# Optimization experiments

Hardware: AMD Instinct MI355X
Metric: run time of the kernel (lower is better)

The kernel has to match this reference:

```python
import jax, jax.numpy as jnp
import numpy as np

L, D, H, FF = 4, 1024, 16, 4096
DH = D // H
EPS = 1e-5


def _ln(x, w, b):
    m = jnp.mean(x, axis=-1, keepdims=True)
    v = jnp.mean(jnp.square(x - m), axis=-1, keepdims=True)
    return (x - m) * jax.lax.rsqrt(v + EPS) * w + b


def setup_inputs() -> dict:
    key = jax.random.key(0)
    ks = jax.random.split(key, 16)
    s = 0.02
    inp = {
        "x": jax.random.normal(ks[0], (2, 2048, D), dtype=jnp.float32),
        "Wq": jax.random.normal(ks[1], (L, D, D), dtype=jnp.float32) * s,
        "Wk": jax.random.normal(ks[2], (L, D, D), dtype=jnp.float32) * s,
        "Wv": jax.random.normal(ks[3], (L, D, D), dtype=jnp.float32) * s,
        "Wo": jax.random.normal(ks[4], (L, D, D), dtype=jnp.float32) * s,
        "bq": jnp.zeros((L, D), jnp.float32),
        "bk": jnp.zeros((L, D), jnp.float32),
        "bv": jnp.zeros((L, D), jnp.float32),
        "bo": jnp.zeros((L, D), jnp.float32),
        "W1": jax.random.normal(ks[5], (L, D, FF), dtype=jnp.float32) * s,
        "b1": jnp.zeros((L, FF), jnp.float32),
        "W2": jax.random.normal(ks[6], (L, FF, D), dtype=jnp.float32) * s,
        "b2": jnp.zeros((L, D), jnp.float32),
        "ln1_w": jnp.ones((L, D), jnp.float32),
        "ln1_b": jnp.zeros((L, D), jnp.float32),
        "ln2_w": jnp.ones((L, D), jnp.float32),
        "ln2_b": jnp.zeros((L, D), jnp.float32),
        "lnf_w": jnp.ones((D,), jnp.float32),
        "lnf_b": jnp.zeros((D,), jnp.float32),
    }
    return inp


def reference(x, Wq, Wk, Wv, Wo, bq, bk, bv, bo, W1, b1, W2, b2,
              ln1_w, ln1_b, ln2_w, ln2_b, lnf_w, lnf_b):
    B, S, _ = x.shape
    scale = 1.0 / jnp.sqrt(jnp.float32(DH))
    for i in range(L):
        # --- pre-norm self-attention (naive math SDPA) ---
        h = _ln(x, ln1_w[i], ln1_b[i])
        q = (h @ Wq[i] + bq[i]).reshape(B, S, H, DH)
        k = (h @ Wk[i] + bk[i]).reshape(B, S, H, DH)
        v = (h @ Wv[i] + bv[i]).reshape(B, S, H, DH)
        scores = jnp.einsum("bqhd,bkhd->bhqk", q, k) * scale  # [B,H,S,S]
        attn = jax.nn.softmax(scores, axis=-1)
        o = jnp.einsum("bhqk,bkhd->bqhd", attn, v).reshape(B, S, D)
        x = x + (o @ Wo[i] + bo[i])
        # --- pre-norm FFN (ReLU) ---
        h2 = _ln(x, ln2_w[i], ln2_b[i])
        x = x + (jax.nn.relu(h2 @ W1[i] + b1[i]) @ W2[i] + b2[i])
    return _ln(x, lnf_w, lnf_b)
```

## Files before the change

kernel.cpp:

```cpp
#include <hip/hip_runtime.h>
#include <cstddef>
#include <cstdint>


#define D_MODEL 1024
#define FF_DIM  4096
#define NTOK    4096
#define SEQ     2048
#define LLAYERS 4

using short8v = __attribute__((ext_vector_type(8))) short;
using f32x16  = __attribute__((ext_vector_type(16))) float;

#define FMA4(a_, s_, b_) { (a_).x += (s_)*(b_).x; (a_).y += (s_)*(b_).y; \
                           (a_).z += (s_)*(b_).z; (a_).w += (s_)*(b_).w; }

__device__ __forceinline__ unsigned short f2bf(float x) {
  unsigned int u = __float_as_uint(x);
  unsigned int r = u + 0x7fffu + ((u >> 16) & 1u);
  return (unsigned short)(r >> 16);
}
__device__ __forceinline__ float bf2f(unsigned short h) {
  return __uint_as_float(((unsigned int)h) << 16);
}
__device__ __forceinline__ void split2(float x, short& hi, short& lo) {
  unsigned short h = f2bf(x);
  hi = (short)h;
  lo = (short)f2bf(x - bf2f(h));
}

__device__ __forceinline__ void gload16(const short* g, short* l) {
  __builtin_amdgcn_global_load_lds(
      (const __attribute__((address_space(1))) unsigned int*)g,
      (__attribute__((address_space(3))) unsigned int*)l, 16, 0, 0);
}

template<int HILO>
__global__ __launch_bounds__(256)
void ln_k(const float* __restrict__ in, const float* __restrict__ w,
          const float* __restrict__ bia, float* __restrict__ outf,
          short* __restrict__ oh, short* __restrict__ ol)
{
  const int wv = threadIdx.x >> 6, lane = threadIdx.x & 63;
  const size_t row = (size_t)blockIdx.x * 4 + wv;
  const float4* x4 = reinterpret_cast<const float4*>(in + row * D_MODEL);
  float4 v[4];
  float s = 0.f;
#pragma unroll
  for (int i = 0; i < 4; i++) {
    v[i] = x4[lane + 64 * i];
    s += v[i].x + v[i].y + v[i].z + v[i].w;
  }
#pragma unroll
  for (int o = 32; o > 0; o >>= 1) s += __shfl_xor(s, o);
  const float mean = s * (1.f / D_MODEL);
  float qv = 0.f;
#pragma unroll
  for (int i = 0; i < 4; i++) {
    float a = v[i].x - mean, b = v[i].y - mean, c = v[i].z - mean, d = v[i].w - mean;
    qv += a * a + b * b + c * c + d * d;
  }
#pragma unroll
  for (int o = 32; o > 0; o >>= 1) qv += __shfl_xor(qv, o);
  const float rstd = rsqrtf(qv * (1.f / D_MODEL) + 1e-5f);
  const float4* w4 = reinterpret_cast<const float4*>(w);
  const float4* b4 = reinterpret_cast<const float4*>(bia);
#pragma unroll
  for (int i = 0; i < 4; i++) {
    float4 ww = w4[lane + 64 * i], bb = b4[lane + 64 * i], r;
    r.x = (v[i].x - mean) * rstd * ww.x + bb.x;
    r.y = (v[i].y - mean) * rstd * ww.y + bb.y;
    r.z = (v[i].z - mean) * rstd * ww.z + bb.z;
    r.w = (v[i].w - mean) * rstd * ww.w + bb.w;
    if (HILO) {
      short4 h, l;
      split2(r.x, h.x, l.x); split2(r.y, h.y, l.y);
      split2(r.z, h.z, l.z); split2(r.w, h.w, l.w);
      size_t off = row * D_MODEL + 4 * lane + 256 * i;
      *reinterpret_cast<short4*>(oh + off) = h;
      *reinterpret_cast<short4*>(ol + off) = l;
    } else {
      reinterpret_cast<float4*>(outf + row * D_MODEL)[lane + 64 * i] = r;
    }
  }
}

struct WPack {
  const float* src[6];
  short* dhi[6];
  short* dlo[6];
  int K[6], N[6];
};
__global__ __launch_bounds__(256)
void cvtw_k(WPack p)
{
  __shared__ float t[32][36];
  const int b = blockIdx.x;
  int m, tile;
  if (b < 4096)      { m = b >> 10; tile = b & 1023; }
  else if (b < 8192) { m = 4; tile = b - 4096; }
  else               { m = 5; tile = b - 8192; }
  const int K = p.K[m], N = p.N[m];
  const int sh = (m == 4) ? 7 : 5;
  const int k0 = (tile >> sh) * 32, n0 = (tile & ((1 << sh) - 1)) * 32;
  const int r = threadIdx.x >> 3, c4 = (threadIdx.x & 7) << 2;
  float4 v = *reinterpret_cast<const float4*>(p.src[m] + (size_t)(k0 + r) * N + n0 + c4);
  *reinterpret_cast<float4*>(&t[r][c4]) = v;
  __syncthreads();
  short4 h, l;
  split2(t[c4 + 0][r], h.x, l.x);
  split2(t[c4 + 1][r], h.y, l.y);
  split2(t[c4 + 2][r], h.z, l.z);
  split2(t[c4 + 3][r], h.w, l.w);
  size_t off = (size_t)(n0 + r) * K + k0 + c4;
  *reinterpret_cast<short4*>(p.dhi[m] + off) = h;
  *reinterpret_cast<short4*>(p.dlo[m] + off) = l;
}

template<int MODE>
__global__ __launch_bounds__(256, 2)
void mgemm_k(const short* __restrict__ Ahg, const short* __restrict__ Alg,
             int K, int Ncols,
             const short* __restrict__ Wh0, const short* __restrict__ Wl0,
             const short* __restrict__ Wh1, const short* __restrict__ Wl1,
             const short* __restrict__ Wh2, const short* __restrict__ Wl2,
             const float* __restrict__ B0, const float* __restrict__ B1,
             const float* __restrict__ B2,
             float* __restrict__ O0, float* __restrict__ O1, float* __restrict__ O2,
             short* __restrict__ OhA, short* __restrict__ OlA,
             short* __restrict__ OhB, short* __restrict__ OlB,
             short* __restrict__ OhC, short* __restrict__ OlC,
             int nbn_per, const float* __restrict__ resid)
{
  __shared__ short Ash0[128 * 64];
  __shared__ short Ash1[128 * 64];
  __shared__ short Bsh0[128 * 64];
  __shared__ short Bsh1[128 * 64];
  const int tid = threadIdx.x;
  const int split = blockIdx.x / nbn_per;
  const int bn = (blockIdx.x % nbn_per) * 128;
  const int bm = blockIdx.y * 128;
  const short* Wh = split == 0 ? Wh0 : (split == 1 ? Wh1 : Wh2);
  const short* Wl = split == 0 ? Wl0 : (split == 1 ? Wl1 : Wl2);
  const float* Bi = split == 0 ? B0 : (split == 1 ? B1 : B2);
  float* Of       = split == 0 ? O0 : (split == 1 ? O1 : O2);
  const int l = tid & 63, w = tid >> 6;
  const int wr = w >> 1, wc = w & 1;

  short* sarr = (w == 0) ? Ash0 : (w == 1) ? Ash1 : (w == 2) ? Bsh0 : Bsh1;
  const short* gbase =
      (w == 0) ? Ahg + (size_t)bm * K :
      (w == 1) ? Alg + (size_t)bm * K :
      (w == 2) ? Wh + (size_t)bn * K :
                 Wl + (size_t)bn * K;
  const int loff = (l >> 3) * K + (((l & 7) ^ (l >> 3)) << 3);

  f32x16 acc[2][2];
#pragma unroll
  for (int a = 0; a < 2; a++)
#pragma unroll
    for (int b = 0; b < 2; b++)
#pragma unroll
      for (int i = 0; i < 16; i++) acc[a][b][i] = 0.f;

  for (int k0 = 0; k0 < K; k0 += 64) {
#pragma unroll
    for (int u = 0; u < 16; u++)
      gload16(gbase + k0 + u * 8 * K + loff, &sarr[u * 512]);
    __syncthreads();
#pragma unroll
    for (int ks = 0; ks < 4; ks++) {
      const int slot = (ks << 1) | (l >> 5);
      short8v afh[2], afl[2], bfh[2], bfl[2];
#pragma unroll
      for (int rt = 0; rt < 2; rt++) {
        int row = wr * 64 + rt * 32 + (l & 31);
        int ia = row * 64 + ((slot ^ (row & 7)) << 3);
        afh[rt] = *reinterpret_cast<const short8v*>(&Ash0[ia]);
        afl[rt] = *reinterpret_cast<const short8v*>(&Ash1[ia]);
        int col = wc * 64 + rt * 32 + (l & 31);
        int ib = col * 64 + ((slot ^ (col & 7)) << 3);
        bfh[rt] = *reinterpret_cast<const short8v*>(&Bsh0[ib]);
        bfl[rt] = *reinterpret_cast<const short8v*>(&Bsh1[ib]);
      }
#pragma unroll
      for (int rt = 0; rt < 2; rt++)
#pragma unroll
        for (int ct = 0; ct < 2; ct++) {
          acc[rt][ct] = __builtin_amdgcn_mfma_f32_32x32x16_bf16(afh[rt], bfh[ct], acc[rt][ct], 0, 0, 0);
          acc[rt][ct] = __builtin_amdgcn_mfma_f32_32x32x16_bf16(afh[rt], bfl[ct], acc[rt][ct], 0, 0, 0);
          acc[rt][ct] = __builtin_amdgcn_mfma_f32_32x32x16_bf16(afl[rt], bfh[ct], acc[rt][ct], 0, 0, 0);
        }
    }
    __syncthreads();
  }

  const int rbase = (l >> 5) * 4, cl = l & 31;
#pragma unroll
  for (int rt = 0; rt < 2; rt++)
#pragma unroll
    for (int ct = 0; ct < 2; ct++) {
      const int colg = bn + wc * 64 + ct * 32 + cl;
      const float bia = Bi[colg];
#pragma unroll
      for (int reg = 0; reg < 16; reg++) {
        const int rowg = bm + wr * 64 + rt * 32 + rbase + (reg & 3) + ((reg >> 2) << 3);
        float v = acc[rt][ct][reg] + bia;
        const size_t off = (size_t)rowg * Ncols + colg;
        if (MODE == 0) {
          Of[off] = v;
        } else if (MODE == 1) {
          Of[off] = v + resid[off];
        } else if (MODE == 2) {
          v = fmaxf(v, 0.f);
          short h, lo; split2(v, h, lo);
          OhA[off] = h; OlA[off] = lo;
        } else {
          short h, lo; split2(v, h, lo);
          if (split < 2) {
            short* OH = split == 0 ? OhA : OhB;
            short* OL = split == 0 ? OlA : OlB;
            OH[off] = h; OL[off] = lo;
          } else {
            const int bbv = rowg >> 11, s = rowg & 2047;
            const int hdv = colg >> 6, dv = colg & 63;
            const int m = s & 15;
            const int pos = (m & 3) + ((m >> 3) << 2) + (((m >> 2) & 1) << 3);
            const size_t voff = ((size_t)(bbv * 16 + hdv) * 64 + dv) * SEQ + (s - m + pos);
            OhC[voff] = h; OlC[voff] = lo;
          }
        }
      }
    }
}

__global__ __launch_bounds__(256)
void mattn_k(const short* __restrict__ qh, const short* __restrict__ ql,
             const short* __restrict__ kh, const short* __restrict__ kl,
             const short* __restrict__ vth, const short* __restrict__ vtl,
             short* __restrict__ oh, short* __restrict__ ol)
{
  __shared__ short Kh[64 * 64], Kl[64 * 64], Vh[64 * 64], Vl[64 * 64];
  const int tid = threadIdx.x;
  const int l = tid & 63, wv = tid >> 6;
  const int lq = l & 31, hb = l >> 5;
  const int qt = blockIdx.x, bh = blockIdx.y;
  const int bb = bh >> 4, hd = bh & 15;

  const size_t qoff = (size_t)(bb * SEQ + qt * 128 + wv * 32 + lq) * D_MODEL + hd * 64 + 8 * hb;
  short8v qfh[4], qfl[4];
#pragma unroll
  for (int c = 0; c < 4; c++) {
    qfh[c] = *reinterpret_cast<const short8v*>(qh + qoff + 16 * c);
    qfl[c] = *reinterpret_cast<const short8v*>(ql + qoff + 16 * c);
  }

  int dst[2];
  size_t kga[2], vga[2];
#pragma unroll
  for (int c = 0; c < 2; c++) {
    int g = tid + c * 256;
    int rr = g >> 3, ss = g & 7;
    dst[c] = rr * 64 + ((ss ^ (rr & 7)) << 3);
    kga[c] = (size_t)(bb * SEQ + rr) * D_MODEL + hd * 64 + ss * 8;
    vga[c] = (size_t)(bh * 64 + rr) * SEQ + ss * 8;
  }
  short8v skh[2], skl[2], svh[2], svl[2];
#pragma unroll
  for (int c = 0; c < 2; c++) {
    skh[c] = *reinterpret_cast<const short8v*>(kh + kga[c]);
    skl[c] = *reinterpret_cast<const short8v*>(kl + kga[c]);
    svh[c] = *reinterpret_cast<const short8v*>(vth + vga[c]);
    svl[c] = *reinterpret_cast<const short8v*>(vtl + vga[c]);
  }

  f32x16 accO[2];
#pragma unroll
  for (int t = 0; t < 2; t++)
#pragma unroll
    for (int i = 0; i < 16; i++) accO[t][i] = 0.f;
  float mrun = -3e38f, lrun = 0.f;

  for (int kt = 0; kt < 32; kt++) {
#pragma unroll
    for (int c = 0; c < 2; c++) {
      *reinterpret_cast<short8v*>(&Kh[dst[c]]) = skh[c];
      *reinterpret_cast<short8v*>(&Kl[dst[c]]) = skl[c];
      *reinterpret_cast<short8v*>(&Vh[dst[c]]) = svh[c];
      *reinterpret_cast<short8v*>(&Vl[dst[c]]) = svl[c];
    }
    __syncthreads();
    if (kt < 31) {
#pragma unroll
      for (int c = 0; c < 2; c++) {
        size_t ko = kga[c] + (size_t)(kt + 1) * 64 * D_MODEL;
        size_t vo = vga[c] + (size_t)(kt + 1) * 64;
        skh[c] = *reinterpret_cast<const short8v*>(kh + ko);
        skl[c] = *reinterpret_cast<const short8v*>(kl + ko);
        svh[c] = *reinterpret_cast<const short8v*>(vth + vo);
        svl[c] = *reinterpret_cast<const short8v*>(vtl + vo);
      }
    }

    f32x16 sc[2];
#pragma unroll
    for (int t = 0; t < 2; t++)
#pragma unroll
      for (int i = 0; i < 16; i++) sc[t][i] = 0.f;
    __builtin_amdgcn_s_setprio(1);
#pragma unroll
    for (int t = 0; t < 2; t++) {
      const int row = 32 * t + lq;
#pragma unroll
      for (int c = 0; c < 4; c++) {
        const int idx = row * 64 + (((2 * c + hb) ^ (row & 7)) << 3);
        short8v ah = *reinterpret_cast<const short8v*>(&Kh[idx]);
        short8v al = *reinterpret_cast<const short8v*>(&Kl[idx]);
        sc[t] = __builtin_amdgcn_mfma_f32_32x32x16_bf16(ah, qfh[c], sc[t], 0, 0, 0);
        sc[t] = __builtin_amdgcn_mfma_f32_32x32x16_bf16(ah, qfl[c], sc[t], 0, 0, 0);
        sc[t] = __builtin_amdgcn_mfma_f32_32x32x16_bf16(al, qfh[c], sc[t], 0, 0, 0);
      }
    }
    __builtin_amdgcn_s_setprio(0);

    float p[2][16];
    float tm = -3e38f;
#pragma unroll
    for (int t = 0; t < 2; t++)
#pragma unroll
      for (int r = 0; r < 16; r++) {
        p[t][r] = sc[t][r] * 0.125f;
        tm = fmaxf(tm, p[t][r]);
      }
    tm = fmaxf(tm, __shfl_xor(tm, 32));
    const float mnew = fmaxf(mrun, tm);
    const float alpha = __expf(mrun - mnew);
    float ps = 0.f;
#pragma unroll
    for (int t = 0; t < 2; t++)
#pragma unroll
      for (int r = 0; r < 16; r++) {
        p[t][r] = __expf(p[t][r] - mnew);
        ps += p[t][r];
      }
    ps += __shfl_xor(ps, 32);
    lrun = lrun * alpha + ps;
    mrun = mnew;
#pragma unroll
    for (int t = 0; t < 2; t++)
#pragma unroll
      for (int i = 0; i < 16; i++) accO[t][i] *= alpha;

    short8v ph[4], pl[4];
#pragma unroll
    for (int c = 0; c < 4; c++) {
#pragma unroll
      for (int j = 0; j < 8; j++) {
        const float v = p[c >> 1][8 * (c & 1) + j];
        const unsigned short hh2 = f2bf(v);
        ph[c][j] = (short)hh2;
        pl[c][j] = (short)f2bf(v - bf2f(hh2));
      }
    }

    __builtin_amdgcn_s_setprio(1);
#pragma unroll
    for (int t = 0; t < 2; t++) {
      const int row = 32 * t + lq;
#pragma unroll
      for (int c = 0; c < 4; c++) {
        const int idx = row * 64 + (((2 * c + hb) ^ (row & 7)) << 3);
        short8v vhf = *reinterpret_cast<const short8v*>(&Vh[idx]);
        short8v vlf = *reinterpret_cast<const short8v*>(&Vl[idx]);
        accO[t] = __builtin_amdgcn_mfma_f32_32x32x16_bf16(vhf, ph[c], accO[t], 0, 0, 0);
        accO[t] = __builtin_amdgcn_mfma_f32_32x32x16_bf16(vhf, pl[c], accO[t], 0, 0, 0);
        accO[t] = __builtin_amdgcn_mfma_f32_32x32x16_bf16(vlf, ph[c], accO[t], 0, 0, 0);
      }
    }
    __builtin_amdgcn_s_setprio(0);
    __syncthreads();
  }

  const float inv = 1.f / lrun;
  const size_t obase = (size_t)(bb * SEQ + qt * 128 + wv * 32 + lq) * D_MODEL + hd * 64;
#pragma unroll
  for (int t = 0; t < 2; t++)
#pragma unroll
    for (int r = 0; r < 16; r++) {
      const int d = 32 * t + (r & 3) + ((r >> 2) << 3) + 4 * hb;
      short hh2, ll2;
      split2(accO[t][r] * inv, hh2, ll2);
      oh[obase + d] = hh2;
      ol[obase + d] = ll2;
    }
}

template<bool RELU, bool RES>
__global__ __launch_bounds__(256)
void gemm_k(const float* __restrict__ A, int K, int Ncols,
            const float* __restrict__ W0, const float* __restrict__ W1p,
            const float* __restrict__ W2p,
            const float* __restrict__ B0, const float* __restrict__ B1p,
            const float* __restrict__ B2p,
            float* __restrict__ O0, float* __restrict__ O1p, float* __restrict__ O2p,
            int nbn_per, const float* __restrict__ resid)
{
  __shared__ float As[16][132];
  __shared__ float Bs[16][132];
  const int tid = threadIdx.x;
  const int split = blockIdx.x / nbn_per;
  const int bn = (blockIdx.x % nbn_per) * 128;
  const int bm = blockIdx.y * 128;
  const float* W  = split == 0 ? W0 : (split == 1 ? W1p : W2p);
  const float* Bi = split == 0 ? B0 : (split == 1 ? B1p : B2p);
  float* O        = split == 0 ? O0 : (split == 1 ? O1p : O2p);
  const int tx = tid & 15, ty = tid >> 4;

  float4 acc[2][4][2];
#pragma unroll
  for (int a = 0; a < 2; a++)
#pragma unroll
    for (int b = 0; b < 4; b++)
#pragma unroll
      for (int c = 0; c < 2; c++) acc[a][b][c] = make_float4(0.f, 0.f, 0.f, 0.f);

  for (int k0 = 0; k0 < K; k0 += 16) {
#pragma unroll
    for (int i = 0; i < 2; i++) {
      int p = tid + i * 256;
      int row = p >> 2, kk4 = (p & 3) << 2;
      float4 va = *reinterpret_cast<const float4*>(A + (size_t)(bm + row) * K + k0 + kk4);
      As[kk4 + 0][row] = va.x; As[kk4 + 1][row] = va.y;
      As[kk4 + 2][row] = va.z; As[kk4 + 3][row] = va.w;
    }
#pragma unroll
    for (int i = 0; i < 2; i++) {
      int p = tid + i * 256;
      int row = p >> 5, c4 = (p & 31) << 2;
      *reinterpret_cast<float4*>(&Bs[row][c4]) =
          *reinterpret_cast<const float4*>(W + (size_t)(k0 + row) * Ncols + bn + c4);
    }
    __syncthreads();
#pragma unroll
    for (int kk = 0; kk < 16; kk++) {
      float4 a0 = *reinterpret_cast<const float4*>(&As[kk][ty * 4]);
      float4 a1 = *reinterpret_cast<const float4*>(&As[kk][64 + ty * 4]);
      float4 b0 = *reinterpret_cast<const float4*>(&Bs[kk][tx * 4]);
      float4 b1 = *reinterpret_cast<const float4*>(&Bs[kk][64 + tx * 4]);
      float av0[4] = {a0.x, a0.y, a0.z, a0.w};
      float av1[4] = {a1.x, a1.y, a1.z, a1.w};
#pragma unroll
      for (int j = 0; j < 4; j++) {
        FMA4(acc[0][j][0], av0[j], b0); FMA4(acc[0][j][1], av0[j], b1);
        FMA4(acc[1][j][0], av1[j], b0); FMA4(acc[1][j][1], av1[j], b1);
      }
    }
    __syncthreads();
  }

#pragma unroll
  for (int ih = 0; ih < 2; ih++)
#pragma unroll
    for (int j = 0; j < 4; j++)
#pragma unroll
      for (int jh = 0; jh < 2; jh++) {
        int row = bm + ih * 64 + ty * 4 + j;
        int col = bn + jh * 64 + tx * 4;
        float4 r = acc[ih][j][jh];
        float4 bb = *reinterpret_cast<const float4*>(Bi + col);
        r.x += bb.x; r.y += bb.y; r.z += bb.z; r.w += bb.w;
        if (RES) {
          float4 rr = *reinterpret_cast<const float4*>(resid + (size_t)row * Ncols + col);
          r.x += rr.x; r.y += rr.y; r.z += rr.z; r.w += rr.w;
        }
        if (RELU) {
          r.x = fmaxf(r.x, 0.f); r.y = fmaxf(r.y, 0.f);
          r.z = fmaxf(r.z, 0.f); r.w = fmaxf(r.w, 0.f);
        }
        *reinterpret_cast<float4*>(O + (size_t)row * Ncols + col) = r;
      }
}

__global__ __launch_bounds__(256)
void attn_k(const float* __restrict__ Q, const float* __restrict__ K,
            const float* __restrict__ V, float* __restrict__ Og)
{
  __shared__ float QsT[64][132];
  __shared__ float KsT[64][68];
  __shared__ float Vs[64][68];
  __shared__ float Ps[128][68];

  const int tid = threadIdx.x, tx = tid & 15, ty = tid >> 4;
  const int bh = blockIdx.y;
  const int bb = bh >> 4, hd = bh & 15;
  const int qt = blockIdx.x;
  const float* Qp = Q + (size_t)(bb * SEQ + qt * 128) * D_MODEL + hd * 64;
  const float* Kp = K + (size_t)(bb * SEQ) * D_MODEL + hd * 64;
  const float* Vp = V + (size_t)(bb * SEQ) * D_MODEL + hd * 64;
  const size_t obase = (size_t)(bb * SEQ + qt * 128) * D_MODEL + hd * 64;

#pragma unroll
  for (int i = 0; i < 8; i++) {
    int p = tid + i * 256;
    int r = p >> 4, k4 = (p & 15) << 2;
    float4 va = *reinterpret_cast<const float4*>(Qp + (size_t)r * D_MODEL + k4);
    QsT[k4 + 0][r] = va.x; QsT[k4 + 1][r] = va.y;
    QsT[k4 + 2][r] = va.z; QsT[k4 + 3][r] = va.w;
  }

  float4 Oa[2][4];
  float mrun[2][4], lrun[2][4];
#pragma unroll
  for (int a = 0; a < 2; a++)
#pragma unroll
    for (int j = 0; j < 4; j++) {
      Oa[a][j] = make_float4(0.f, 0.f, 0.f, 0.f);
      mrun[a][j] = -1e30f; lrun[a][j] = 0.f;
    }

  __syncthreads();

  for (int kt = 0; kt < 32; kt++) {
#pragma unroll
    for (int i = 0; i < 4; i++) {
      int p = tid + i * 256;
      int r = p >> 4, k4 = (p & 15) << 2;
      float4 kv = *reinterpret_cast<const float4*>(Kp + (size_t)(kt * 64 + r) * D_MODEL + k4);
      KsT[k4 + 0][r] = kv.x; KsT[k4 + 1][r] = kv.y;
      KsT[k4 + 2][r] = kv.z; KsT[k4 + 3][r] = kv.w;
      float4 vv = *reinterpret_cast<const float4*>(Vp + (size_t)(kt * 64 + r) * D_MODEL + k4);
      *reinterpret_cast<float4*>(&Vs[r][k4]) = vv;
    }
    __syncthreads();

    float4 sc[2][4];
#pragma unroll
    for (int a = 0; a < 2; a++)
#pragma unroll
      for (int j = 0; j < 4; j++) sc[a][j] = make_float4(0.f, 0.f, 0.f, 0.f);

#pragma unroll 8
    for (int kk = 0; kk < 64; kk++) {
      float4 b0 = *reinterpret_cast<const float4*>(&KsT[kk][tx * 4]);
      float4 a0 = *reinterpret_cast<const float4*>(&QsT[kk][ty * 4]);
      float4 a1 = *reinterpret_cast<const float4*>(&QsT[kk][64 + ty * 4]);
      float av0[4] = {a0.x, a0.y, a0.z, a0.w};
      float av1[4] = {a1.x, a1.y, a1.z, a1.w};
#pragma unroll
      for (int j = 0; j < 4; j++) {
        FMA4(sc[0][j], av0[j], b0);
        FMA4(sc[1][j], av1[j], b0);
      }
    }

#pragma unroll
    for (int a = 0; a < 2; a++)
#pragma unroll
      for (int j = 0; j < 4; j++) {
        float4 s4 = sc[a][j];
        s4.x *= 0.125f; s4.y *= 0.125f; s4.z *= 0.125f; s4.w *= 0.125f;
        float tm = fmaxf(fmaxf(s4.x, s4.y), fmaxf(s4.z, s4.w));
#pragma unroll
        for (int o = 8; o > 0; o >>= 1) tm = fmaxf(tm, __shfl_xor(tm, o));
        float mnew = fmaxf(mrun[a][j], tm);
        float alpha = __expf(mrun[a][j] - mnew);
        float4 p;
        p.x = __expf(s4.x - mnew); p.y = __expf(s4.y - mnew);
        p.z = __expf(s4.z - mnew); p.w = __expf(s4.w - mnew);
        float ps = p.x + p.y + p.z + p.w;
#pragma unroll
        for (int o = 8; o > 0; o >>= 1) ps += __shfl_xor(ps, o);
        lrun[a][j] = lrun[a][j] * alpha + ps;
        mrun[a][j] = mnew;
        Oa[a][j].x *= alpha; Oa[a][j].y *= alpha;
        Oa[a][j].z *= alpha; Oa[a][j].w *= alpha;
        *reinterpret_cast<float4*>(&Ps[a * 64 + ty * 4 + j][tx * 4]) = p;
      }
    __syncthreads();

#pragma unroll 4
    for (int k4 = 0; k4 < 16; k4++) {
      float4 b[4];
#pragma unroll
      for (int u = 0; u < 4; u++)
        b[u] = *reinterpret_cast<const float4*>(&Vs[k4 * 4 + u][tx * 4]);
#pragma unroll
      for (int a = 0; a < 2; a++)
#pragma unroll
        for (int j = 0; j < 4; j++) {
          float4 p = *reinterpret_cast<const float4*>(&Ps[a * 64 + ty * 4 + j][k4 * 4]);
          FMA4(Oa[a][j], p.x, b[0]);
          FMA4(Oa[a][j], p.y, b[1]);
          FMA4(Oa[a][j], p.z, b[2]);
          FMA4(Oa[a][j], p.w, b[3]);
        }
    }
    __syncthreads();
  }

#pragma unroll
  for (int a = 0; a < 2; a++)
#pragma unroll
    for (int j = 0; j < 4; j++) {
      float inv = 1.f / lrun[a][j];
      float4 r = Oa[a][j];
      r.x *= inv; r.y *= inv; r.z *= inv; r.w *= inv;
      *reinterpret_cast<float4*>(Og + obase + (size_t)(a * 64 + ty * 4 + j) * D_MODEL + tx * 4) = r;
    }
}

extern "C" void kernel_launch(void* const* d_in, const int* in_sizes, int n_in,
                              void* d_out, int out_size, void* d_ws, size_t ws_size,
                              hipStream_t stream)
{
  (void)in_sizes; (void)n_in; (void)out_size;
  const float* x    = (const float*)d_in[0];
  const float* Wq   = (const float*)d_in[1];
  const float* Wk   = (const float*)d_in[2];
  const float* Wv   = (const float*)d_in[3];
  const float* Wo   = (const float*)d_in[4];
  const float* bq   = (const float*)d_in[5];
  const float* bk   = (const float*)d_in[6];
  const float* bv   = (const float*)d_in[7];
  const float* bo   = (const float*)d_in[8];
  const float* W1   = (const float*)d_in[9];
  const float* b1   = (const float*)d_in[10];
  const float* W2   = (const float*)d_in[11];
  const float* b2   = (const float*)d_in[12];
  const float* ln1w = (const float*)d_in[13];
  const float* ln1b = (const float*)d_in[14];
  const float* ln2w = (const float*)d_in[15];
  const float* ln2b = (const float*)d_in[16];
  const float* lnfw = (const float*)d_in[17];
  const float* lnfb = (const float*)d_in[18];

  const size_t ND = (size_t)NTOK * D_MODEL;
  const size_t M1 = 1024 * 1024;
  float* xb = (float*)d_out;

  hipMemcpyAsync(xb, x, sizeof(float) * ND, hipMemcpyDeviceToDevice, stream);

  const size_t REQ_MFMA = 184549376;
  const bool use_mfma = (ws_size >= REQ_MFMA);

  if (use_mfma) {
    short* wT_h = (short*)d_ws;
    short* wT_l = wT_h + 12 * M1;
    short* h_hi = wT_l + 12 * M1;
    short* h_lo = h_hi + ND;
    short* q_hi = h_lo + ND;
    short* q_lo = q_hi + ND;
    short* k_hi = q_lo + ND;
    short* k_lo = k_hi + ND;
    short* vT_h = k_lo + ND;
    short* vT_l = vT_h + ND;
    short* t_hi = vT_l + ND;
    short* t_lo = t_hi + (size_t)NTOK * FF_DIM;

    for (int i = 0; i < LLAYERS; i++) {
      WPack p;
      p.src[0] = Wq + (size_t)i * M1; p.src[1] = Wk + (size_t)i * M1;
      p.src[2] = Wv + (size_t)i * M1; p.src[3] = Wo + (size_t)i * M1;
      p.src[4] = W1 + (size_t)i * D_MODEL * FF_DIM;
      p.src[5] = W2 + (size_t)i * FF_DIM * D_MODEL;
      for (int m = 0; m < 6; m++) {
        static const size_t doff[6] = {0, M1, 2 * M1, 3 * M1, 4 * M1, 8 * M1};
        p.dhi[m] = wT_h + doff[m]; p.dlo[m] = wT_l + doff[m];
      }
      p.K[0] = p.K[1] = p.K[2] = p.K[3] = 1024; p.K[4] = 1024; p.K[5] = 4096;
      p.N[0] = p.N[1] = p.N[2] = p.N[3] = 1024; p.N[4] = 4096; p.N[5] = 1024;
      cvtw_k<<<12288, 256, 0, stream>>>(p);

      ln_k<1><<<NTOK / 4, 256, 0, stream>>>(xb, ln1w + (size_t)i * D_MODEL,
                                            ln1b + (size_t)i * D_MODEL, nullptr, h_hi, h_lo);
      mgemm_k<3><<<dim3(24, 32), 256, 0, stream>>>(
          h_hi, h_lo, 1024, 1024,
          wT_h, wT_l, wT_h + M1, wT_l + M1, wT_h + 2 * M1, wT_l + 2 * M1,
          bq + (size_t)i * D_MODEL, bk + (size_t)i * D_MODEL, bv + (size_t)i * D_MODEL,
          nullptr, nullptr, nullptr,
          q_hi, q_lo, k_hi, k_lo, vT_h, vT_l, 8, nullptr);
      mattn_k<<<dim3(16, 32), 256, 0, stream>>>(q_hi, q_lo, k_hi, k_lo, vT_h, vT_l, h_hi, h_lo);
      mgemm_k<1><<<dim3(8, 32), 256, 0, stream>>>(
          h_hi, h_lo, 1024, 1024,
          wT_h + 3 * M1, wT_l + 3 * M1, wT_h + 3 * M1, wT_l + 3 * M1, wT_h + 3 * M1, wT_l + 3 * M1,
          bo + (size_t)i * D_MODEL, bo + (size_t)i * D_MODEL, bo + (size_t)i * D_MODEL,
          xb, xb, xb,
          nullptr, nullptr, nullptr, nullptr, nullptr, nullptr, 8, xb);
      ln_k<1><<<NTOK / 4, 256, 0, stream>>>(xb, ln2w + (size_t)i * D_MODEL,
                                            ln2b + (size_t)i * D_MODEL, nullptr, h_hi, h_lo);
      mgemm_k<2><<<dim3(32, 32), 256, 0, stream>>>(
          h_hi, h_lo, 1024, 4096,
          wT_h + 4 * M1, wT_l + 4 * M1, wT_h + 4 * M1, wT_l + 4 * M1, wT_h + 4 * M1, wT_l + 4 * M1,
          b1 + (size_t)i * FF_DIM, b1 + (size_t)i * FF_DIM, b1 + (size_t)i * FF_DIM,
          nullptr, nullptr, nullptr,
          t_hi, t_lo, nullptr, nullptr, nullptr, nullptr, 32, nullptr);
      mgemm_k<1><<<dim3(8, 32), 256, 0, stream>>>(
          t_hi, t_lo, 4096, 1024,
          wT_h + 8 * M1, wT_l + 8 * M1, wT_h + 8 * M1, wT_l + 8 * M1, wT_h + 8 * M1, wT_l + 8 * M1,
          b2 + (size_t)i * D_MODEL, b2 + (size_t)i * D_MODEL, b2 + (size_t)i * D_MODEL,
          xb, xb, xb,
          nullptr, nullptr, nullptr, nullptr, nullptr, nullptr, 8, xb);
    }
    ln_k<0><<<NTOK / 4, 256, 0, stream>>>(xb, lnfw, lnfb, xb, nullptr, nullptr);
    return;
  }

  float* h  = (float*)d_ws;
  float* qb = h + ND;
  float* kb = qb + ND;
  float* vb = kb + ND;
  float* tb = qb;

  for (int i = 0; i < LLAYERS; i++) {
    const float* Wq_l = Wq + (size_t)i * M1;
    const float* Wk_l = Wk + (size_t)i * M1;
    const float* Wv_l = Wv + (size_t)i * M1;
    const float* Wo_l = Wo + (size_t)i * M1;
    const float* W1_l = W1 + (size_t)i * D_MODEL * FF_DIM;
    const float* W2_l = W2 + (size_t)i * FF_DIM * D_MODEL;

    ln_k<0><<<NTOK / 4, 256, 0, stream>>>(xb, ln1w + (size_t)i * D_MODEL,
                                          ln1b + (size_t)i * D_MODEL, h, nullptr, nullptr);
    gemm_k<false, false><<<dim3(24, 32), 256, 0, stream>>>(
        h, D_MODEL, D_MODEL, Wq_l, Wk_l, Wv_l,
        bq + (size_t)i * D_MODEL, bk + (size_t)i * D_MODEL, bv + (size_t)i * D_MODEL,
        qb, kb, vb, 8, nullptr);
    attn_k<<<dim3(16, 32), 256, 0, stream>>>(qb, kb, vb, h);
    gemm_k<false, true><<<dim3(8, 32), 256, 0, stream>>>(
        h, D_MODEL, D_MODEL, Wo_l, Wo_l, Wo_l,
        bo + (size_t)i * D_MODEL, bo + (size_t)i * D_MODEL, bo + (size_t)i * D_MODEL,
        xb, xb, xb, 8, xb);
    ln_k<0><<<NTOK / 4, 256, 0, stream>>>(xb, ln2w + (size_t)i * D_MODEL,
                                          ln2b + (size_t)i * D_MODEL, h, nullptr, nullptr);
    gemm_k<true, false><<<dim3(32, 32), 256, 0, stream>>>(
        h, D_MODEL, FF_DIM, W1_l, W1_l, W1_l,
        b1 + (size_t)i * FF_DIM, b1 + (size_t)i * FF_DIM, b1 + (size_t)i * FF_DIM,
        tb, tb, tb, 32, nullptr);
    gemm_k<false, true><<<dim3(8, 32), 256, 0, stream>>>(
        tb, FF_DIM, D_MODEL, W2_l, W2_l, W2_l,
        b2 + (size_t)i * D_MODEL, b2 + (size_t)i * D_MODEL, b2 + (size_t)i * D_MODEL,
        xb, xb, xb, 8, xb);
  }
  ln_k<0><<<NTOK / 4, 256, 0, stream>>>(xb, lnfw, lnfb, xb, nullptr, nullptr);
}
```

Before: 2.293 ms.

## Double-buffer GEMM LDS, swizzle tile order, lazy softmax rescale with exp2 and fewer PV MFMAs

The GEMM kernel gets double-buffered shared memory so the next K-tile's global loads overlap the current MFMAs. Occupancy drops to one block per CU and workgroups are remapped into a swizzled order for better cache locality. The scale and log2(e) are folded into Q at the projection epilogue, so attention uses exp2 directly. Attention also skips the rescale unless the running max grows by more than 8, and drops the P-low split MFMA in the PV product. This cuts exp and MFMA work but lowers the precision of P and changes occupancy.

```diff
diff --git a/kernel.cpp b/kernel.cpp
--- a/kernel.cpp
+++ b/kernel.cpp
@@ -8,6 +8,7 @@
 #define NTOK    4096
 #define SEQ     2048
 #define LLAYERS 4
+#define QSCALE  0.180336880111f
 
 using short8v = __attribute__((ext_vector_type(8))) short;
 using f32x16  = __attribute__((ext_vector_type(16))) float;
@@ -118,7 +119,7 @@
 }
 
 template<int MODE>
-__global__ __launch_bounds__(256, 2)
+__global__ __launch_bounds__(256, 1)
 void mgemm_k(const short* __restrict__ Ahg, const short* __restrict__ Alg,
              int K, int Ncols,
              const short* __restrict__ Wh0, const short* __restrict__ Wl0,
@@ -132,14 +133,18 @@
              short* __restrict__ OhC, short* __restrict__ OlC,
              int nbn_per, const float* __restrict__ resid)
 {
-  __shared__ short Ash0[128 * 64];
-  __shared__ short Ash1[128 * 64];
-  __shared__ short Bsh0[128 * 64];
-  __shared__ short Bsh1[128 * 64];
+  __shared__ short buf[2][4][128 * 64];
   const int tid = threadIdx.x;
-  const int split = blockIdx.x / nbn_per;
-  const int bn = (blockIdx.x % nbn_per) * 128;
-  const int bm = blockIdx.y * 128;
+
+  const int gx = gridDim.x;
+  const int nwg = gx * gridDim.y;
+  const int g = blockIdx.y * gx + blockIdx.x;
+  const int lg = (g & 7) * (nwg >> 3) + (g >> 3);
+  const int bxs = lg % gx, bys = lg / gx;
+
+  const int split = bxs / nbn_per;
+  const int bn = (bxs % nbn_per) * 128;
+  const int bm = bys * 128;
   const short* Wh = split == 0 ? Wh0 : (split == 1 ? Wh1 : Wh2);
   const short* Wl = split == 0 ? Wl0 : (split == 1 ? Wl1 : Wl2);
   const float* Bi = split == 0 ? B0 : (split == 1 ? B1 : B2);
@@ -147,7 +152,6 @@
   const int l = tid & 63, w = tid >> 6;
   const int wr = w >> 1, wc = w & 1;
 
-  short* sarr = (w == 0) ? Ash0 : (w == 1) ? Ash1 : (w == 2) ? Bsh0 : Bsh1;
   const short* gbase =
       (w == 0) ? Ahg + (size_t)bm * K :
       (w == 1) ? Alg + (size_t)bm * K :
@@ -163,11 +167,26 @@
 #pragma unroll
       for (int i = 0; i < 16; i++) acc[a][b][i] = 0.f;
 
-  for (int k0 = 0; k0 < K; k0 += 64) {
-#pragma unroll
-    for (int u = 0; u < 16; u++)
-      gload16(gbase + k0 + u * 8 * K + loff, &sarr[u * 512]);
+  const int nt = K >> 6;
+  {
+    const short* g0 = gbase + loff;
+    short* s0 = &buf[0][w][0];
+#pragma unroll
+    for (int u = 0; u < 16; u++) gload16(g0 + u * 8 * K, s0 + u * 512);
+  }
+  int p = 0;
+  for (int t = 0; t < nt; ++t) {
     __syncthreads();
+    if (t + 1 < nt) {
+      const short* g0 = gbase + ((t + 1) << 6) + loff;
+      short* s0 = &buf[p ^ 1][w][0];
+#pragma unroll
+      for (int u = 0; u < 16; u++) gload16(g0 + u * 8 * K, s0 + u * 512);
+    }
+    const short* Ah = &buf[p][0][0];
+    const short* Al = &buf[p][1][0];
+    const short* Bh = &buf[p][2][0];
+    const short* Bl = &buf[p][3][0];
 #pragma unroll
     for (int ks = 0; ks < 4; ks++) {
       const int slot = (ks << 1) | (l >> 5);
@@ -176,12 +195,12 @@
       for (int rt = 0; rt < 2; rt++) {
         int row = wr * 64 + rt * 32 + (l & 31);
         int ia = row * 64 + ((slot ^ (row & 7)) << 3);
-        afh[rt] = *reinterpret_cast<const short8v*>(&Ash0[ia]);
-        afl[rt] = *reinterpret_cast<const short8v*>(&Ash1[ia]);
+        afh[rt] = *reinterpret_cast<const short8v*>(&Ah[ia]);
+        afl[rt] = *reinterpret_cast<const short8v*>(&Al[ia]);
         int col = wc * 64 + rt * 32 + (l & 31);
         int ib = col * 64 + ((slot ^ (col & 7)) << 3);
-        bfh[rt] = *reinterpret_cast<const short8v*>(&Bsh0[ib]);
-        bfl[rt] = *reinterpret_cast<const short8v*>(&Bsh1[ib]);
+        bfh[rt] = *reinterpret_cast<const short8v*>(&Bh[ib]);
+        bfl[rt] = *reinterpret_cast<const short8v*>(&Bl[ib]);
       }
 #pragma unroll
       for (int rt = 0; rt < 2; rt++)
@@ -192,7 +211,7 @@
           acc[rt][ct] = __builtin_amdgcn_mfma_f32_32x32x16_bf16(afl[rt], bfh[ct], acc[rt][ct], 0, 0, 0);
         }
     }
-    __syncthreads();
+    p ^= 1;
   }
 
   const int rbase = (l >> 5) * 4, cl = l & 31;
@@ -216,6 +235,7 @@
           short h, lo; split2(v, h, lo);
           OhA[off] = h; OlA[off] = lo;
         } else {
+          if (split == 0) v *= QSCALE;
           short h, lo; split2(v, h, lo);
           if (split < 2) {
             short* OH = split == 0 ? OhA : OhB;
@@ -323,45 +343,40 @@
     }
     __builtin_amdgcn_s_setprio(0);
 
+    float tm = -3e38f;
+#pragma unroll
+    for (int t = 0; t < 2; t++)
+#pragma unroll
+      for (int r = 0; r < 16; r++) tm = fmaxf(tm, sc[t][r]);
+    tm = fmaxf(tm, __shfl_xor(tm, 32));
+    if (__any(tm - mrun > 8.f)) {
+      const float mnew = fmaxf(mrun, tm);
+      const float al = exp2f(mrun - mnew);
+      lrun *= al;
+#pragma unroll
+      for (int t = 0; t < 2; t++)
+#pragma unroll
+        for (int i = 0; i < 16; i++) accO[t][i] *= al;
+      mrun = mnew;
+    }
     float p[2][16];
-    float tm = -3e38f;
+    float ps = 0.f;
 #pragma unroll
     for (int t = 0; t < 2; t++)
 #pragma unroll
       for (int r = 0; r < 16; r++) {
-        p[t][r] = sc[t][r] * 0.125f;
-        tm = fmaxf(tm, p[t][r]);
-      }
-    tm = fmaxf(tm, __shfl_xor(tm, 32));
-    const float mnew = fmaxf(mrun, tm);
-    const float alpha = __expf(mrun - mnew);
-    float ps = 0.f;
-#pragma unroll
-    for (int t = 0; t < 2; t++)
-#pragma unroll
-      for (int r = 0; r < 16; r++) {
-        p[t][r] = __expf(p[t][r] - mnew);
+        p[t][r] = exp2f(sc[t][r] - mrun);
         ps += p[t][r];
       }
     ps += __shfl_xor(ps, 32);
-    lrun = lrun * alpha + ps;
-    mrun = mnew;
-#pragma unroll
-    for (int t = 0; t < 2; t++)
-#pragma unroll
-      for (int i = 0; i < 16; i++) accO[t][i] *= alpha;
-
-    short8v ph[4], pl[4];
-#pragma unroll
-    for (int c = 0; c < 4; c++) {
-#pragma unroll
-      for (int j = 0; j < 8; j++) {
-        const float v = p[c >> 1][8 * (c & 1) + j];
-        const unsigned short hh2 = f2bf(v);
-        ph[c][j] = (short)hh2;
-        pl[c][j] = (short)f2bf(v - bf2f(hh2));
-      }
-    }
+    lrun += ps;
+
+    short8v ph[4];
+#pragma unroll
+    for (int c = 0; c < 4; c++)
+#pragma unroll
+      for (int j = 0; j < 8; j++)
+        ph[c][j] = (short)f2bf(p[c >> 1][8 * (c & 1) + j]);
 
     __builtin_amdgcn_s_setprio(1);
 #pragma unroll
@@ -373,7 +388,6 @@
         short8v vhf = *reinterpret_cast<const short8v*>(&Vh[idx]);
         short8v vlf = *reinterpret_cast<const short8v*>(&Vl[idx]);
         accO[t] = __builtin_amdgcn_mfma_f32_32x32x16_bf16(vhf, ph[c], accO[t], 0, 0, 0);
-        accO[t] = __builtin_amdgcn_mfma_f32_32x32x16_bf16(vhf, pl[c], accO[t], 0, 0, 0);
         accO[t] = __builtin_amdgcn_mfma_f32_32x32x16_bf16(vlf, ph[c], accO[t], 0, 0, 0);
       }
     }
```

Result: faster. 2.234 ms (-2.6%).
